# Performance work log

Hardware: AMD Instinct MI355X
Metric: run time of the kernel (lower is better)

The kernel has to match this reference:

```python
import jax, jax.numpy as jnp
import numpy as np

LORA_ALPHA = 16.0
TOP_K = 2


def setup_inputs() -> dict:
    key = jax.random.key(0)
    k_x, k_w, k_g, k_a, k_b = jax.random.split(key, 5)
    B, S, H, O, E, R = 2, 2048, 2048, 2048, 8, 16
    x = jax.random.normal(k_x, (B, S, H), dtype=jnp.float32)
    weight = jax.random.normal(k_w, (O, H), dtype=jnp.float32)          # frozen base W [out, in]
    gate_w = jax.random.normal(k_g, (E, H), dtype=jnp.float32) * 0.02   # router gate [E, in]
    A_w = jax.random.normal(k_a, (E, R, H), dtype=jnp.float32) * (1.0 / np.sqrt(H))  # stacked lora_A
    B_w = jax.random.normal(k_b, (E, O, R), dtype=jnp.float32) * 0.01   # stacked lora_B
    return {"x": x, "weight": weight, "gate_w": gate_w, "A_w": A_w, "B_w": B_w}


def reference(x, weight, gate_w, A_w, B_w):
    E = gate_w.shape[0]
    # Base frozen linear: F.linear(x, weight)
    out = jnp.einsum("bsh,oh->bso", x, weight)

    # Router: softmax over experts, top-2, renormalize
    logits = jnp.einsum("bsh,eh->bse", x, gate_w)
    probs = jax.nn.softmax(logits, axis=-1)
    topk_w, topk_idx = jax.lax.top_k(probs, TOP_K)          # [b,s,2]
    topk_w = topk_w / jnp.sum(topk_w, axis=-1, keepdims=True)

    # Per-token combine weight for each expert (sum over the 2 slots)
    onehot = jax.nn.one_hot(topk_idx, E, dtype=x.dtype)      # [b,s,2,E]
    cw = jnp.einsum("bsk,bske->bse", topk_w, onehot)         # [b,s,E]

    # LoRA: down-project into all experts' rank spaces, weight, then up-project.
    # t: [b,s,E,r] is small (r=16); weighting here avoids a [b,s,E,out] buffer.
    t = jnp.einsum("bsh,erh->bser", x, A_w)
    t = t * cw[..., None]
    lora = jnp.einsum("bser,eor->bso", t, B_w)

    return out + LORA_ALPHA * lora
```

## Files before the change

kernel.cpp:

```cpp
#include <hip/hip_runtime.h>
#include <hip/hip_bf16.h>


typedef __bf16 bf16x8 __attribute__((ext_vector_type(8)));
typedef float f32x4 __attribute__((ext_vector_type(4)));

__device__ __forceinline__ __bf16 f2bf(float f) {
  union { float f; unsigned u; } v; v.f = f;
  unsigned r = (v.u + 0x7FFFu + ((v.u >> 16) & 1u)) >> 16;
  unsigned short s = (unsigned short)r;
  return __builtin_bit_cast(__bf16, s);
}

__device__ __forceinline__ void ld_lds16(const void* g, void* l) {
  __builtin_amdgcn_global_load_lds((__attribute__((address_space(1))) void*)g,
                                   (__attribute__((address_space(3))) void*)l,
                                   16, 0, 0);
}

__global__ void prep_kernel(const float* __restrict__ W, const float* __restrict__ Aw,
                            const float* __restrict__ Bw, __bf16* __restrict__ Bfull,
                            __bf16* __restrict__ A2) {
  const int b = blockIdx.x, tid = threadIdx.x;
  if (b < 2176) {
    const float* src = (b < 2048) ? (W + (size_t)b * 2048)
                                  : (Aw + (size_t)(b - 2048) * 2048);
    __bf16* dst = (b < 2048) ? (Bfull + (size_t)b * 2176)
                             : (A2 + (size_t)(b - 2048) * 2048);
    const int c = tid * 8;
    float4 a = *(const float4*)(src + c);
    float4 d = *(const float4*)(src + c + 4);
    bf16x8 v;
    v[0] = f2bf(a.x); v[1] = f2bf(a.y); v[2] = f2bf(a.z); v[3] = f2bf(a.w);
    v[4] = f2bf(d.x); v[5] = f2bf(d.y); v[6] = f2bf(d.z); v[7] = f2bf(d.w);
    *(bf16x8*)(dst + c) = v;
  } else {
    const int idx = (b - 2176) * 256 + tid;
    const int e = idx >> 11, o = idx & 2047;
    const float4* s = (const float4*)(Bw + ((size_t)e * 2048 + o) * 16);
    float4 v0 = s[0], v1 = s[1], v2 = s[2], v3 = s[3];
    __bf16* d = Bfull + (size_t)o * 2176 + 2048 + e * 16;
    bf16x8 lo, hi;
    lo[0] = f2bf(v0.x); lo[1] = f2bf(v0.y); lo[2] = f2bf(v0.z); lo[3] = f2bf(v0.w);
    lo[4] = f2bf(v1.x); lo[5] = f2bf(v1.y); lo[6] = f2bf(v1.z); lo[7] = f2bf(v1.w);
    hi[0] = f2bf(v2.x); hi[1] = f2bf(v2.y); hi[2] = f2bf(v2.z); hi[3] = f2bf(v2.w);
    hi[4] = f2bf(v3.x); hi[5] = f2bf(v3.y); hi[6] = f2bf(v3.z); hi[7] = f2bf(v3.w);
    *(bf16x8*)d = lo;
    *(bf16x8*)(d + 8) = hi;
  }
}

__global__ __launch_bounds__(256) void router_kernel(
    const float* __restrict__ x, const float* __restrict__ gw,
    __bf16* __restrict__ Abuf, float* __restrict__ cw) {
  __shared__ float gws[8 * 2048];
  __shared__ float red[8][4][8];
  const int tid = threadIdx.x;
  const int wave = tid >> 6, lane = tid & 63;
  for (int i = tid; i < 4096; i += 256) ((float4*)gws)[i] = ((const float4*)gw)[i];
  __syncthreads();

  const int t0 = blockIdx.x * 8;
  const int c = tid * 8;
  for (int tk = 0; tk < 8; ++tk) {
    const int t = t0 + tk;
    const float* xr = x + (size_t)t * 2048;
    float4 v0 = *(const float4*)(xr + c);
    float4 v1 = *(const float4*)(xr + c + 4);
    float xs[8] = {v0.x, v0.y, v0.z, v0.w, v1.x, v1.y, v1.z, v1.w};
    bf16x8 bv;
#pragma unroll
    for (int j = 0; j < 8; ++j) bv[j] = f2bf(xs[j]);
    *(bf16x8*)(Abuf + (size_t)t * 2176 + c) = bv;

    float acc[8] = {0, 0, 0, 0, 0, 0, 0, 0};
#pragma unroll
    for (int j = 0; j < 8; ++j) {
      const float xv = xs[j];
#pragma unroll
      for (int e = 0; e < 8; ++e) acc[e] += xv * gws[e * 2048 + c + j];
    }
#pragma unroll
    for (int e = 0; e < 8; ++e)
      for (int off = 32; off; off >>= 1) acc[e] += __shfl_down(acc[e], off);
    if (lane == 0) {
#pragma unroll
      for (int e = 0; e < 8; ++e) red[tk][wave][e] = acc[e];
    }
  }
  __syncthreads();
  if (tid < 8) {
    const int tk = tid, t = t0 + tk;
    float lg[8];
#pragma unroll
    for (int e = 0; e < 8; ++e)
      lg[e] = red[tk][0][e] + red[tk][1][e] + red[tk][2][e] + red[tk][3][e];
    int a = 0;
    for (int e = 1; e < 8; ++e) if (lg[e] > lg[a]) a = e;
    int b = (a == 0) ? 1 : 0;
    for (int e = 0; e < 8; ++e) if (e != a && lg[e] > lg[b]) b = e;
    const float d = __expf(lg[b] - lg[a]);
    const float wa = 1.0f / (1.0f + d), wb = d / (1.0f + d);
    float o[8] = {0, 0, 0, 0, 0, 0, 0, 0};
    o[a] = wa; o[b] = wb;
#pragma unroll
    for (int e = 0; e < 8; ++e) cw[t * 8 + e] = o[e];
  }
}

__global__ void t2_finish(const float* __restrict__ tpart, const float* __restrict__ cw,
                          __bf16* __restrict__ Abuf) {
  const int idx = blockIdx.x * 256 + threadIdx.x;
  const int t = idx >> 7, k2 = idx & 127;
  float s = tpart[idx] + tpart[idx + 524288] + tpart[idx + 2 * 524288] +
            tpart[idx + 3 * 524288];
  const float w = cw[t * 8 + (k2 >> 4)] * 16.0f;
  Abuf[(size_t)t * 2176 + 2048 + k2] = f2bf(s * w);
}

__global__ __launch_bounds__(256) void mfma_gemm_bt(
    const __bf16* __restrict__ A, const __bf16* __restrict__ B,
    float* __restrict__ C, int lda, int ldb, int ldc, int kiters,
    long long czstride) {
  __shared__ __align__(16) __bf16 As[128 * 64];
  __shared__ __align__(16) __bf16 Bs[128 * 64];
  const int tid = threadIdx.x;
  const int wave = tid >> 6;
  const int lane = tid & 63;
  const int tm = blockIdx.x * 128;
  const int tn = blockIdx.y * 128;
  C += (long long)blockIdx.z * czstride;

  const int wm = (wave >> 1) * 64;
  const int wn = (wave & 1) * 64;
  const int srow = lane >> 3;
  const int skoff = ((lane & 7) ^ srow) * 8;

  const int rlo = lane & 7;
  const int rb3 = (lane >> 3) & 1;
  const int qb = lane >> 4;

  f32x4 acc[4][4] = {};

  int kcur = blockIdx.z * kiters * 64;
  for (int kt = 0; kt < kiters; ++kt) {
#pragma unroll
    for (int r = 0; r < 4; ++r) {
      const int ch = r * 4 + wave;
      ld_lds16(A + (size_t)(tm + ch * 8 + srow) * lda + kcur + skoff, &As[ch * 512]);
      ld_lds16(B + (size_t)(tn + ch * 8 + srow) * ldb + kcur + skoff, &Bs[ch * 512]);
    }
    __syncthreads();
#pragma unroll
    for (int ks = 0; ks < 2; ++ks) {
      bf16x8 af[4], bfg[4];
#pragma unroll
      for (int i = 0; i < 4; ++i) {
        const int rh = ((wm + i * 16) >> 3) + rb3;
        const int q = (ks * 4 + qb) ^ rlo;
        af[i] = *(const bf16x8*)&As[rh * 512 + rlo * 64 + q * 8];
      }
#pragma unroll
      for (int j = 0; j < 4; ++j) {
        const int rh = ((wn + j * 16) >> 3) + rb3;
        const int q = (ks * 4 + qb) ^ rlo;
        bfg[j] = *(const bf16x8*)&Bs[rh * 512 + rlo * 64 + q * 8];
      }
#pragma unroll
      for (int i = 0; i < 4; ++i)
#pragma unroll
        for (int j = 0; j < 4; ++j)
          acc[i][j] = __builtin_amdgcn_mfma_f32_16x16x32_bf16(af[i], bfg[j], acc[i][j], 0, 0, 0);
    }
    __syncthreads();
    kcur += 64;
  }

  const int crow0 = tm + wm + (lane >> 4) * 4;
  const int ccol0 = tn + wn + (lane & 15);
#pragma unroll
  for (int i = 0; i < 4; ++i)
#pragma unroll
    for (int j = 0; j < 4; ++j)
#pragma unroll
      for (int rg = 0; rg < 4; ++rg)
        C[(size_t)(crow0 + i * 16 + rg) * ldc + ccol0 + j * 16] = acc[i][j][rg];
}

extern "C" void kernel_launch(void* const* d_in, const int* in_sizes, int n_in,
                              void* d_out, int out_size, void* d_ws, size_t ws_size,
                              hipStream_t stream) {
  const float* x = (const float*)d_in[0];
  const float* weight = (const float*)d_in[1];
  const float* gate_w = (const float*)d_in[2];
  const float* A_w = (const float*)d_in[3];
  const float* B_w = (const float*)d_in[4];
  float* out = (float*)d_out;

  char* ws = (char*)d_ws;
  __bf16* Abuf = (__bf16*)ws;
  __bf16* Bfull = (__bf16*)(ws + 17825792);
  __bf16* A2 = (__bf16*)(ws + 26738688);
  float* tpart = (float*)(ws + 27262976);
  float* cw = (float*)(ws + 35651584);

  prep_kernel<<<2240, 256, 0, stream>>>(weight, A_w, B_w, Bfull, A2);
  router_kernel<<<512, 256, 0, stream>>>(x, gate_w, Abuf, cw);
  mfma_gemm_bt<<<dim3(32, 1, 4), 256, 0, stream>>>(Abuf, A2, tpart, 2176, 2048, 128,
                                                   8, 524288LL);
  t2_finish<<<2048, 256, 0, stream>>>(tpart, cw, Abuf);
  mfma_gemm_bt<<<dim3(32, 16, 1), 256, 0, stream>>>(Abuf, Bfull, out, 2176, 2176,
                                                    2048, 34, 0LL);
}
```

Baseline: 174.5 us.

## Fuse router and LoRA down-projection into one kernel; retile main GEMM to 128x64

Merges the router, the split-K LoRA down-projection GEMM and its finish kernel into a single router_t2 kernel. It stages 16 bf16 tokens in LDS, computes the gate logits and top-2 weights, then runs MFMA against A2 and writes the scaled LoRA activations straight into Abuf. This removes two launches and the fp32 partial-sum buffer round trip. Separately, the main GEMM moves to 128-thread blocks with 128x64 tiles and launch_bounds(128,2), doubling the grid to 1024 blocks. That may improve occupancy or tail behaviour but halves B-tile reuse per block.

New measurement: 166.5 us. 1.05x faster.

```diff
diff --git a/kernel.cpp b/kernel.cpp
--- a/kernel.cpp
+++ b/kernel.cpp
@@ -50,89 +50,109 @@
   }
 }
 
-__global__ __launch_bounds__(256) void router_kernel(
+__global__ __launch_bounds__(256) void router_t2(
     const float* __restrict__ x, const float* __restrict__ gw,
-    __bf16* __restrict__ Abuf, float* __restrict__ cw) {
-  __shared__ float gws[8 * 2048];
-  __shared__ float red[8][4][8];
+    const __bf16* __restrict__ A2, __bf16* __restrict__ Abuf) {
+  __shared__ __align__(16) __bf16 xs[16][2056];
+  __shared__ float red[4][16][8];
+  __shared__ float cws[16][8];
   const int tid = threadIdx.x;
   const int wave = tid >> 6, lane = tid & 63;
-  for (int i = tid; i < 4096; i += 256) ((float4*)gws)[i] = ((const float4*)gw)[i];
+  const int t0 = blockIdx.x * 16;
+
+#pragma unroll 4
+  for (int i = 0; i < 16; ++i) {
+    const float* xr = x + (size_t)(t0 + i) * 2048 + tid * 8;
+    float4 a = *(const float4*)xr;
+    float4 b = *(const float4*)(xr + 4);
+    bf16x8 v;
+    v[0] = f2bf(a.x); v[1] = f2bf(a.y); v[2] = f2bf(a.z); v[3] = f2bf(a.w);
+    v[4] = f2bf(b.x); v[5] = f2bf(b.y); v[6] = f2bf(b.z); v[7] = f2bf(b.w);
+    *(bf16x8*)(Abuf + (size_t)(t0 + i) * 2176 + tid * 8) = v;
+    *(bf16x8*)&xs[i][tid * 8] = v;
+  }
   __syncthreads();
 
-  const int t0 = blockIdx.x * 8;
-  const int c = tid * 8;
-  for (int tk = 0; tk < 8; ++tk) {
-    const int t = t0 + tk;
-    const float* xr = x + (size_t)t * 2048;
-    float4 v0 = *(const float4*)(xr + c);
-    float4 v1 = *(const float4*)(xr + c + 4);
-    float xs[8] = {v0.x, v0.y, v0.z, v0.w, v1.x, v1.y, v1.z, v1.w};
-    bf16x8 bv;
-#pragma unroll
-    for (int j = 0; j < 8; ++j) bv[j] = f2bf(xs[j]);
-    *(bf16x8*)(Abuf + (size_t)t * 2176 + c) = bv;
-
-    float acc[8] = {0, 0, 0, 0, 0, 0, 0, 0};
-#pragma unroll
-    for (int j = 0; j < 8; ++j) {
-      const float xv = xs[j];
-#pragma unroll
-      for (int e = 0; e < 8; ++e) acc[e] += xv * gws[e * 2048 + c + j];
-    }
+  const int tok = tid & 15, slc = tid >> 4;
+  const int c0 = slc * 128;
+  float acc[8] = {0, 0, 0, 0, 0, 0, 0, 0};
+  for (int j8 = 0; j8 < 16; ++j8) {
+    bf16x8 xv = *(const bf16x8*)&xs[tok][c0 + j8 * 8];
+    float xf[8];
+#pragma unroll
+    for (int j = 0; j < 8; ++j) xf[j] = (float)xv[j];
+#pragma unroll
+    for (int e = 0; e < 8; ++e) {
+      float4 g0 = *(const float4*)(gw + e * 2048 + c0 + j8 * 8);
+      float4 g1 = *(const float4*)(gw + e * 2048 + c0 + j8 * 8 + 4);
+      acc[e] += xf[0] * g0.x + xf[1] * g0.y + xf[2] * g0.z + xf[3] * g0.w +
+                xf[4] * g1.x + xf[5] * g1.y + xf[6] * g1.z + xf[7] * g1.w;
+    }
+  }
+#pragma unroll
+  for (int e = 0; e < 8; ++e) {
+    acc[e] += __shfl_down(acc[e], 16);
+    acc[e] += __shfl_down(acc[e], 32);
+  }
+  if (lane < 16) {
+#pragma unroll
+    for (int e = 0; e < 8; ++e) red[wave][lane][e] = acc[e];
+  }
+  __syncthreads();
+  if (tid < 16) {
+    float lg[8];
 #pragma unroll
     for (int e = 0; e < 8; ++e)
-      for (int off = 32; off; off >>= 1) acc[e] += __shfl_down(acc[e], off);
-    if (lane == 0) {
-#pragma unroll
-      for (int e = 0; e < 8; ++e) red[tk][wave][e] = acc[e];
-    }
-  }
-  __syncthreads();
-  if (tid < 8) {
-    const int tk = tid, t = t0 + tk;
-    float lg[8];
-#pragma unroll
-    for (int e = 0; e < 8; ++e)
-      lg[e] = red[tk][0][e] + red[tk][1][e] + red[tk][2][e] + red[tk][3][e];
+      lg[e] = red[0][tid][e] + red[1][tid][e] + red[2][tid][e] + red[3][tid][e];
     int a = 0;
     for (int e = 1; e < 8; ++e) if (lg[e] > lg[a]) a = e;
     int b = (a == 0) ? 1 : 0;
     for (int e = 0; e < 8; ++e) if (e != a && lg[e] > lg[b]) b = e;
     const float d = __expf(lg[b] - lg[a]);
-    const float wa = 1.0f / (1.0f + d), wb = d / (1.0f + d);
     float o[8] = {0, 0, 0, 0, 0, 0, 0, 0};
-    o[a] = wa; o[b] = wb;
-#pragma unroll
-    for (int e = 0; e < 8; ++e) cw[t * 8 + e] = o[e];
-  }
-}
-
-__global__ void t2_finish(const float* __restrict__ tpart, const float* __restrict__ cw,
-                          __bf16* __restrict__ Abuf) {
-  const int idx = blockIdx.x * 256 + threadIdx.x;
-  const int t = idx >> 7, k2 = idx & 127;
-  float s = tpart[idx] + tpart[idx + 524288] + tpart[idx + 2 * 524288] +
-            tpart[idx + 3 * 524288];
-  const float w = cw[t * 8 + (k2 >> 4)] * 16.0f;
-  Abuf[(size_t)t * 2176 + 2048 + k2] = f2bf(s * w);
-}
-
-__global__ __launch_bounds__(256) void mfma_gemm_bt(
+    o[a] = 1.0f / (1.0f + d);
+    o[b] = d / (1.0f + d);
+#pragma unroll
+    for (int e = 0; e < 8; ++e) cws[tid][e] = o[e];
+  }
+  __syncthreads();
+
+  const int m = lane & 15, q = lane >> 4;
+  const int nt0 = wave * 2;
+  f32x4 tacc[2] = {};
+  for (int ks = 0; ks < 64; ++ks) {
+    bf16x8 af = *(const bf16x8*)&xs[m][ks * 32 + q * 8];
+#pragma unroll
+    for (int h = 0; h < 2; ++h) {
+      bf16x8 bfg = *(const bf16x8*)(A2 + (size_t)((nt0 + h) * 16 + m) * 2048 +
+                                    ks * 32 + q * 8);
+      tacc[h] = __builtin_amdgcn_mfma_f32_16x16x32_bf16(af, bfg, tacc[h], 0, 0, 0);
+    }
+  }
+#pragma unroll
+  for (int h = 0; h < 2; ++h) {
+    const int nt = nt0 + h;
+#pragma unroll
+    for (int rg = 0; rg < 4; ++rg) {
+      const int trow = q * 4 + rg;
+      const float s = tacc[h][rg] * 16.0f * cws[trow][nt];
+      Abuf[(size_t)(t0 + trow) * 2176 + 2048 + nt * 16 + m] = f2bf(s);
+    }
+  }
+}
+
+__global__ __launch_bounds__(128, 2) void mfma_gemm_bt(
     const __bf16* __restrict__ A, const __bf16* __restrict__ B,
-    float* __restrict__ C, int lda, int ldb, int ldc, int kiters,
-    long long czstride) {
+    float* __restrict__ C, int lda, int ldb, int ldc, int kiters) {
   __shared__ __align__(16) __bf16 As[128 * 64];
-  __shared__ __align__(16) __bf16 Bs[128 * 64];
+  __shared__ __align__(16) __bf16 Bs[64 * 64];
   const int tid = threadIdx.x;
   const int wave = tid >> 6;
   const int lane = tid & 63;
   const int tm = blockIdx.x * 128;
-  const int tn = blockIdx.y * 128;
-  C += (long long)blockIdx.z * czstride;
-
-  const int wm = (wave >> 1) * 64;
-  const int wn = (wave & 1) * 64;
+  const int tn = blockIdx.y * 64;
+
+  const int wm = wave * 64;
   const int srow = lane >> 3;
   const int skoff = ((lane & 7) ^ srow) * 8;
 
@@ -142,29 +162,32 @@
 
   f32x4 acc[4][4] = {};
 
-  int kcur = blockIdx.z * kiters * 64;
+  int kcur = 0;
   for (int kt = 0; kt < kiters; ++kt) {
 #pragma unroll
+    for (int r = 0; r < 8; ++r) {
+      const int ch = r * 2 + wave;
+      ld_lds16(A + (size_t)(tm + ch * 8 + srow) * lda + kcur + skoff, &As[ch * 512]);
+    }
+#pragma unroll
     for (int r = 0; r < 4; ++r) {
-      const int ch = r * 4 + wave;
-      ld_lds16(A + (size_t)(tm + ch * 8 + srow) * lda + kcur + skoff, &As[ch * 512]);
+      const int ch = r * 2 + wave;
       ld_lds16(B + (size_t)(tn + ch * 8 + srow) * ldb + kcur + skoff, &Bs[ch * 512]);
     }
     __syncthreads();
 #pragma unroll
     for (int ks = 0; ks < 2; ++ks) {
       bf16x8 af[4], bfg[4];
+      const int q8 = ((ks * 4 + qb) ^ rlo) * 8;
 #pragma unroll
       for (int i = 0; i < 4; ++i) {
         const int rh = ((wm + i * 16) >> 3) + rb3;
-        const int q = (ks * 4 + qb) ^ rlo;
-        af[i] = *(const bf16x8*)&As[rh * 512 + rlo * 64 + q * 8];
+        af[i] = *(const bf16x8*)&As[rh * 512 + rlo * 64 + q8];
       }
 #pragma unroll
       for (int j = 0; j < 4; ++j) {
-        const int rh = ((wn + j * 16) >> 3) + rb3;
-        const int q = (ks * 4 + qb) ^ rlo;
-        bfg[j] = *(const bf16x8*)&Bs[rh * 512 + rlo * 64 + q * 8];
+        const int rh = ((j * 16) >> 3) + rb3;
+        bfg[j] = *(const bf16x8*)&Bs[rh * 512 + rlo * 64 + q8];
       }
 #pragma unroll
       for (int i = 0; i < 4; ++i)
@@ -177,7 +200,7 @@
   }
 
   const int crow0 = tm + wm + (lane >> 4) * 4;
-  const int ccol0 = tn + wn + (lane & 15);
+  const int ccol0 = tn + (lane & 15);
 #pragma unroll
   for (int i = 0; i < 4; ++i)
 #pragma unroll
@@ -201,14 +224,9 @@
   __bf16* Abuf = (__bf16*)ws;
   __bf16* Bfull = (__bf16*)(ws + 17825792);
   __bf16* A2 = (__bf16*)(ws + 26738688);
-  float* tpart = (float*)(ws + 27262976);
-  float* cw = (float*)(ws + 35651584);
 
   prep_kernel<<<2240, 256, 0, stream>>>(weight, A_w, B_w, Bfull, A2);
-  router_kernel<<<512, 256, 0, stream>>>(x, gate_w, Abuf, cw);
-  mfma_gemm_bt<<<dim3(32, 1, 4), 256, 0, stream>>>(Abuf, A2, tpart, 2176, 2048, 128,
-                                                   8, 524288LL);
-  t2_finish<<<2048, 256, 0, stream>>>(tpart, cw, Abuf);
-  mfma_gemm_bt<<<dim3(32, 16, 1), 256, 0, stream>>>(Abuf, Bfull, out, 2176, 2176,
-                                                    2048, 34, 0LL);
-}
+  router_t2<<<256, 256, 0, stream>>>(x, gate_w, A2, Abuf);
+  mfma_gemm_bt<<<dim3(32, 32), 128, 0, stream>>>(Abuf, Bfull, out, 2176, 2176,
+                                                 2048, 34);
+}
```
